# Kernel tuning notes

Measured on AMD Instinct MI355X. Metric: run time of the kernel, lower is better.

Reference implementation:

```python
import jax, jax.numpy as jnp
import numpy as np

B, S, HS = 2, 2048, 4096
NH, NKV = 32, 32
HD = HS // NH
INTER = 11008
VOCAB = 32000
EPS = 1e-6
ROPE_BASE = 10000.0


def setup_inputs() -> dict:
    key = jax.random.key(0)
    ks = jax.random.split(key, 16)
    sc = 0.02
    return {
        "hidden_states": jax.random.normal(ks[0], (B, S, HS), jnp.float32),
        "input_ids": jax.random.randint(ks[1], (B, S), 0, VOCAB, jnp.int32),
        "position_ids": jnp.arange(S, dtype=jnp.int32)[None, :],
        "embed": jax.random.normal(ks[2], (VOCAB, HS), jnp.float32) * sc,
        "fc_w": jax.random.normal(ks[3], (HS, 2 * HS), jnp.float32) * sc,
        "fc_b": jnp.zeros((HS,), jnp.float32),
        "q_w": jax.random.normal(ks[4], (NH * HD, HS), jnp.float32) * sc,
        "k_w": jax.random.normal(ks[5], (NKV * HD, HS), jnp.float32) * sc,
        "v_w": jax.random.normal(ks[6], (NKV * HD, HS), jnp.float32) * sc,
        "o_w": jax.random.normal(ks[7], (HS, NH * HD), jnp.float32) * sc,
        "gate_w": jax.random.normal(ks[8], (INTER, HS), jnp.float32) * sc,
        "up_w": jax.random.normal(ks[9], (INTER, HS), jnp.float32) * sc,
        "down_w": jax.random.normal(ks[10], (HS, INTER), jnp.float32) * sc,
        "post_ln_w": jnp.ones((HS,), jnp.float32),
    }


def _rotate_half(x):
    x1, x2 = jnp.split(x, 2, axis=-1)
    return jnp.concatenate((-x2, x1), axis=-1)


def _rms_norm(x, w, eps=EPS):
    x32 = x.astype(jnp.float32)
    x32 = x32 * jax.lax.rsqrt(jnp.mean(x32 * x32, axis=-1, keepdims=True) + eps)
    return (w * x32).astype(x.dtype)


def _forward(hidden_states, input_ids, position_ids, embed, fc_w, fc_b,
             q_w, k_w, v_w, o_w, gate_w, up_w, down_w, post_ln_w):
    # Embedding lookup (detached in original via no_grad)
    embeds = jax.lax.stop_gradient(embed[input_ids])  # [B,S,HS]
    h = jnp.concatenate((embeds, hidden_states), axis=-1) @ fc_w.T + fc_b  # [B,S,HS]

    # --- decoder layer 0 (no input_layernorm) ---
    residual = h
    q = (h @ q_w.T).reshape(B, S, NH, HD).transpose(0, 2, 1, 3)   # [B,NH,S,HD]
    k = (h @ k_w.T).reshape(B, S, NKV, HD).transpose(0, 2, 1, 3)
    v = (h @ v_w.T).reshape(B, S, NKV, HD).transpose(0, 2, 1, 3)

    # RoPE
    pos = position_ids[0].astype(jnp.float32)                      # [S]
    inv_freq = 1.0 / (ROPE_BASE ** (jnp.arange(0, HD, 2, dtype=jnp.float32) / HD))
    freqs = pos[:, None] * inv_freq[None, :]                       # [S,HD/2]
    emb = jnp.concatenate((freqs, freqs), axis=-1)                 # [S,HD]
    cos = jnp.cos(emb)[None, None, :, :]
    sin = jnp.sin(emb)[None, None, :, :]
    q = q * cos + _rotate_half(q) * sin
    k = k * cos + _rotate_half(k) * sin

    # attention (num_kv_groups == 1 here)
    scores = jnp.einsum('bhqd,bhkd->bhqk', q, k) / np.sqrt(HD)     # [B,NH,S,S]
    causal = jnp.triu(jnp.ones((S, S), bool), 1)
    scores = jnp.where(causal[None, None], -jnp.inf, scores)
    attn = jax.nn.softmax(scores.astype(jnp.float32), axis=-1).astype(q.dtype)
    out = jnp.einsum('bhqk,bhkd->bhqd', attn, v)                   # [B,NH,S,HD]
    out = out.transpose(0, 2, 1, 3).reshape(B, S, HS)
    attn_out = out @ o_w.T

    h = residual + attn_out
    residual = h
    hn = _rms_norm(h, post_ln_w)
    mlp = (jax.nn.silu(hn @ gate_w.T) * (hn @ up_w.T)) @ down_w.T
    return residual + mlp


def reference(hidden_states, input_ids, position_ids, embed, fc_w, fc_b,
              q_w, k_w, v_w, o_w, gate_w, up_w, down_w, post_ln_w):
    return _forward(hidden_states, input_ids, position_ids, embed, fc_w, fc_b,
                    q_w, k_w, v_w, o_w, gate_w, up_w, down_w, post_ln_w)
```

## Files before the change

### kernel.cpp

```cpp
#include <hip/hip_runtime.h>
#include <hip/hip_bf16.h>

typedef __attribute__((ext_vector_type(8))) short short8;
typedef __attribute__((ext_vector_type(4))) short short4v;
typedef __attribute__((ext_vector_type(4))) float floatx4;

#define B_SZ 2
#define S_SZ 2048
#define HS_SZ 4096
#define NH_SZ 32
#define HD_SZ 128
#define INTER_SZ 11008
#define M_TOT 4096
#define QKV_N 12288
#define GU_N 22016

__device__ __forceinline__ float b2f(short s){
  unsigned int u = ((unsigned int)(unsigned short)s) << 16;
  return __builtin_bit_cast(float, u);
}
__device__ __forceinline__ short f2b(float f){
  unsigned int u = __builtin_bit_cast(unsigned int, f);
  u = (u + 0x7FFFu + ((u >> 16) & 1u)) >> 16;
  return (short)u;
}

typedef __attribute__((address_space(1))) const unsigned int gu32;
typedef __attribute__((address_space(3))) unsigned int lu32;
__device__ __forceinline__ void gl2lds16(const short* g, short* l){
  __builtin_amdgcn_global_load_lds((gu32*)g, (lu32*)l, 16, 0, 0);
}

#define BARRIER() asm volatile("s_barrier" ::: "memory")
#define WAITV8()  asm volatile("s_waitcnt vmcnt(8)" ::: "memory")
#define WAITV4()  asm volatile("s_waitcnt vmcnt(4)" ::: "memory")
#define WAITV2()  asm volatile("s_waitcnt vmcnt(2)" ::: "memory")
#define WAITV0()  asm volatile("s_waitcnt vmcnt(0)" ::: "memory")

__global__ void cvt_bf16_kernel(const float* __restrict__ src, short* __restrict__ dst, long n8){
  long idx = (long)blockIdx.x * blockDim.x + threadIdx.x;
  if (idx >= n8) return;
  long e = idx * 8;
  floatx4 v0 = *(const floatx4*)(src + e);
  floatx4 v1 = *(const floatx4*)(src + e + 4);
  short8 o;
  o[0]=f2b(v0[0]); o[1]=f2b(v0[1]); o[2]=f2b(v0[2]); o[3]=f2b(v0[3]);
  o[4]=f2b(v1[0]); o[5]=f2b(v1[1]); o[6]=f2b(v1[2]); o[7]=f2b(v1[3]);
  *(short8*)(dst + e) = o;
}

__global__ void embed_concat_kernel(const float* __restrict__ hidden,
                                    const int* __restrict__ ids,
                                    const float* __restrict__ embed,
                                    short* __restrict__ X0){
  long idx = (long)blockIdx.x * blockDim.x + threadIdx.x;
  const long total = (long)M_TOT * (2*HS_SZ) / 4;
  if (idx >= total) return;
  long e = idx * 4;
  int m = (int)(e / (2*HS_SZ));
  int c = (int)(e % (2*HS_SZ));
  const float* src;
  if (c < HS_SZ){
    src = embed + (long)ids[m]*HS_SZ + c;
  } else {
    src = hidden + (long)m*HS_SZ + (c - HS_SZ);
  }
  floatx4 v = *(const floatx4*)src;
  short4v o;
  o[0]=f2b(v[0]); o[1]=f2b(v[1]); o[2]=f2b(v[2]); o[3]=f2b(v[3]);
  *(short4v*)(X0 + e) = o;
}

#define G_STAGE(op,h,kof,qb) { \
  gl2lds16(gs[op][h] + (kof), lds + (qb) + (op)*16384 + (h)*8192 + wid*1024); \
  gl2lds16(gs[op][h] + k8o[op] + (kof), lds + (qb) + (op)*16384 + (h)*8192 + wid*1024 + 512); }

#define LD_A(Mh,pb) { \
  _Pragma("unroll") \
  for (int mf=0; mf<4; mf++) \
    _Pragma("unroll") \
    for (int ks=0; ks<2; ks++) \
      af[mf][ks] = *(const short8*)(lds + (pb) + ((Mh)*128 + wr2*64 + mf*16 + lr)*64 + (((ks*4+lk)^lr7))*8); }

#define LD_B(BB,Nh,pb) { \
  _Pragma("unroll") \
  for (int nf=0; nf<2; nf++) \
    _Pragma("unroll") \
    for (int ks=0; ks<2; ks++) \
      BB[nf][ks] = *(const short8*)(lds + (pb) + 16384 + ((Nh)*128 + wc2*32 + nf*16 + lr)*64 + (((ks*4+lk)^lr7))*8); }

#define MMQ(Mh,Nh,BB) { \
  __builtin_amdgcn_s_setprio(1); \
  _Pragma("unroll") \
  for (int mf=0; mf<4; mf++) \
    _Pragma("unroll") \
    for (int nf=0; nf<2; nf++){ \
      acc[Mh][Nh][mf][nf] = __builtin_amdgcn_mfma_f32_16x16x32_bf16(af[mf][0], BB[nf][0], acc[Mh][Nh][mf][nf], 0,0,0); \
      acc[Mh][Nh][mf][nf] = __builtin_amdgcn_mfma_f32_16x16x32_bf16(af[mf][1], BB[nf][1], acc[Mh][Nh][mf][nf], 0,0,0); \
    } \
  __builtin_amdgcn_s_setprio(0); }

template<int EPI>
__global__ __launch_bounds__(512, 2)
void gemm256_kernel(const short* __restrict__ A, const short* __restrict__ Bw,
                    const short* __restrict__ Bw2, int nsplit,
                    int K, int lda, int ldc,
                    const float* __restrict__ bias,
                    const short* __restrict__ residb,
                    short* __restrict__ Cbf,
                    float* __restrict__ Cf){
  __shared__ __align__(16) short lds[65536];
  const int tid = threadIdx.x;
  const int wid = tid >> 6;
  const int lane = tid & 63;
  const int wr2 = wid >> 2, wc2 = wid & 3;
  const int lr = lane & 15, lk = lane >> 4;
  const int lr7 = lr & 7;

  const int nwg = gridDim.x * gridDim.y;
  const int id  = blockIdx.y * gridDim.x + blockIdx.x;
  const int cpx = nwg >> 3;
  const int sw  = (id & 7) * cpx + (id >> 3);
  const int bx  = sw % gridDim.x;
  const int by  = sw / gridDim.x;
  const int m0 = bx * 256, n0 = by * 256;

  const int srow = lane >> 3;
  const int sslot = (lane & 7) ^ srow;
  const long k8o[2] = { 8L * lda, 8L * K };
  const short* gs[2][2];
  #pragma unroll
  for (int h=0; h<2; h++){
    const int rowa = m0 + h*128 + wid*16 + srow;
    gs[0][h] = A + (long)rowa*lda + sslot*8;
    const int rowb = n0 + h*128 + wid*16 + srow;
    gs[1][h] = (rowb < nsplit ? Bw + (long)rowb*K
                              : Bw2 + (long)(rowb - nsplit)*K) + sslot*8;
  }

  floatx4 acc[2][2][4][2] = {};
  short8 af[4][2], b0[2][2], b1[2][2];
  const int nt = K >> 6;

  G_STAGE(0,0,0,0); G_STAGE(1,0,0,0); G_STAGE(1,1,0,0); G_STAGE(0,1,0,0);
  WAITV4(); BARRIER();

  for (int t = 0; t < nt-1; ++t){
    const int pb = (t & 1) << 15;
    const int qb = pb ^ 32768;
    const long kof = (long)(t+1) * 64;
    LD_A(0,pb); LD_B(b0,0,pb);
    G_STAGE(0,0,kof,qb);
    BARRIER();
    MMQ(0,0,b0);
    WAITV4(); BARRIER();
    LD_B(b1,1,pb);
    G_STAGE(1,0,kof,qb);
    BARRIER();
    MMQ(0,1,b1);
    WAITV4(); BARRIER();
    LD_A(1,pb);
    G_STAGE(1,1,kof,qb);
    BARRIER();
    MMQ(1,1,b1);
    BARRIER();
    G_STAGE(0,1,kof,qb);
    BARRIER();
    MMQ(1,0,b0);
    WAITV4(); BARRIER();
  }
  {
    const int pb = ((nt-1) & 1) << 15;
    LD_A(0,pb); LD_B(b0,0,pb);
    BARRIER(); MMQ(0,0,b0);
    WAITV2(); BARRIER();
    LD_B(b1,1,pb);
    BARRIER(); MMQ(0,1,b1);
    WAITV0(); BARRIER();
    LD_A(1,pb);
    BARRIER(); MMQ(1,1,b1);
    BARRIER();
    MMQ(1,0,b0);
  }

  #pragma unroll
  for (int Mh=0; Mh<2; Mh++){
    #pragma unroll
    for (int Nh=0; Nh<2; Nh++){
      #pragma unroll
      for (int mf=0; mf<4; mf++){
        #pragma unroll
        for (int nf=0; nf<2; nf++){
          const int col = n0 + Nh*128 + wc2*32 + nf*16 + lr;
          float bcol = (EPI==1) ? bias[col] : 0.0f;
          #pragma unroll
          for (int r=0; r<4; r++){
            const int row = m0 + Mh*128 + wr2*64 + mf*16 + lk*4 + r;
            float v = acc[Mh][Nh][mf][nf][r] + bcol;
            if (EPI==2 || EPI==3) v += b2f(residb[(long)row*ldc + col]);
            if (EPI==3) Cf[(long)row*ldc + col] = v;
            else        Cbf[(long)row*ldc + col] = f2b(v);
          }
        }
      }
    }
  }
}

__global__ void rope_kernel(short* __restrict__ qkv, const int* __restrict__ pos_ids){
  long idx = (long)blockIdx.x * blockDim.x + threadIdx.x;
  const long total = (long)M_TOT * NH_SZ * (HD_SZ/2);
  if (idx >= total) return;
  int i  = (int)(idx & 63);
  long rh = idx >> 6;
  int h  = (int)(rh & 31);
  int m  = (int)(rh >> 5);
  int s  = m & (S_SZ - 1);
  float p = (float)pos_ids[s];
  const float L2_10000 = 13.28771237954945f;
  float inv = exp2f(-(2.0f*i/(float)HD_SZ) * L2_10000);
  float fr = p * inv;
  float sn, cs;
  sincosf(fr, &sn, &cs);
  short* qp = qkv + (long)m*QKV_N + h*HD_SZ;
  short* kp = qp + HS_SZ;
  float q1=b2f(qp[i]), q2=b2f(qp[i+64]);
  qp[i]    = f2b(q1*cs - q2*sn);
  qp[i+64] = f2b(q2*cs + q1*sn);
  float k1=b2f(kp[i]), k2=b2f(kp[i+64]);
  kp[i]    = f2b(k1*cs - k2*sn);
  kp[i+64] = f2b(k2*cs + k1*sn);
}

__global__ __launch_bounds__(256)
void vtrans_kernel(const short* __restrict__ QKV, short* __restrict__ VT){
  __shared__ short tile[64][68];
  const int s0 = blockIdx.x * 64;
  const int d0 = blockIdx.y * 64;
  const int bh = blockIdx.z;
  const int b = bh >> 5, h = bh & 31;
  const int tid = threadIdx.x;
  #pragma unroll
  for (int it=0; it<2; it++){
    int e = (it*256 + tid) * 8;
    int ss = e >> 6, col = e & 63;
    short8 v = *(const short8*)(QKV + ((long)(b*S_SZ + s0 + ss))*QKV_N + 2*HS_SZ + h*HD_SZ + d0 + col);
    #pragma unroll
    for (int j=0;j<8;j++) tile[ss][col+j] = v[j];
  }
  __syncthreads();
  #pragma unroll
  for (int it=0; it<2; it++){
    int e = (it*256 + tid) * 8;
    int dd = e >> 6, scol = e & 63;
    short8 w;
    #pragma unroll
    for (int j=0;j<8;j++) w[j] = tile[scol+j][dd];
    *(short8*)(VT + ((long)(bh*HD_SZ + d0 + dd))*S_SZ + s0 + scol) = w;
  }
}

__global__ __launch_bounds__(512,1)
void attn_kernel(const short* __restrict__ QKV, const short* __restrict__ VT,
                 short* __restrict__ O){
  constexpr int LPD = 72;
  __shared__ __align__(16) short lds[32768];
  __shared__ __align__(16) short p_lds[8][16*LPD];
  const int bh = blockIdx.y;
  const int b = bh >> 5, h = bh & 31;
  const int qblk = blockIdx.x * 128;
  const int tid = threadIdx.x, wid = tid>>6, lane = tid&63;
  const int lr = lane & 15, lk = lane >> 4;
  const float scale = 0.08838834764831845f;

  const short* qbase = QKV + ((long)(b*S_SZ + qblk + wid*16))*QKV_N + h*HD_SZ;
  short8 qf[4];
  #pragma unroll
  for (int t=0;t<4;t++)
    qf[t] = *(const short8*)(qbase + (long)lr*QKV_N + t*32 + lk*8);

  const short* kb[2]; const short* vb[2];
  int kloff[2], vloff[2];
  #pragma unroll
  for (int p=0;p<2;p++){
    const int i = wid*2 + p;
    const int rowk = i*4 + (lane >> 4);
    const int slotk = (lane & 15) ^ (rowk & 15);
    kb[p] = QKV + ((long)(b*S_SZ) + rowk)*QKV_N + HS_SZ + h*HD_SZ + slotk*8;
    kloff[p] = i*512;
    const int dv = i*8 + (lane >> 3);
    const int slotv = (lane & 7) ^ (dv & 7);
    vb[p] = VT + ((long)(bh*HD_SZ + dv))*S_SZ + slotv*8;
    vloff[p] = 8192 + i*512;
  }

  floatx4 oacc[8] = {};
  float m_run[4] = {-1e30f,-1e30f,-1e30f,-1e30f};
  float l_run[4] = {0.f,0.f,0.f,0.f};

  const int nt = 2*(blockIdx.x + 1);

  #pragma unroll
  for (int p=0;p<2;p++){
    gl2lds16(kb[p], lds + kloff[p]);
    gl2lds16(vb[p], lds + vloff[p]);
  }

  for (int t=0; t<nt; ++t){
    const int dbase = (t & 1) * 16384;
    const int nbase = ((t+1) & 1) * 16384;
    if (t+1 < nt){
      const long kkn = (long)(t+1)*64*QKV_N;
      const long vkn = (long)(t+1)*64;
      #pragma unroll
      for (int p=0;p<2;p++){
        gl2lds16(kb[p] + kkn, lds + nbase + kloff[p]);
        gl2lds16(vb[p] + vkn, lds + nbase + vloff[p]);
      }
      WAITV4();
    } else {
      WAITV0();
    }
    BARRIER();
    const int kv0 = t*64;
    floatx4 sfr[4];
    __builtin_amdgcn_s_setprio(1);
    #pragma unroll
    for (int fn=0; fn<4; fn++){
      floatx4 s = {0.f,0.f,0.f,0.f};
      const int row = fn*16 + lr;
      #pragma unroll
      for (int tq=0; tq<4; tq++){
        short8 kf = *(const short8*)(lds + dbase + row*128 + (((tq*4+lk)^lr)&15)*8);
        s = __builtin_amdgcn_mfma_f32_16x16x32_bf16(qf[tq], kf, s, 0,0,0);
      }
      sfr[fn] = s;
    }
    __builtin_amdgcn_s_setprio(0);
    float pv[4][4];
    #pragma unroll
    for (int fn=0; fn<4; fn++){
      const int col = kv0 + fn*16 + lr;
      #pragma unroll
      for (int r=0;r<4;r++){
        const int row = qblk + wid*16 + lk*4 + r;
        float sv = sfr[fn][r] * scale;
        pv[fn][r] = (col > row) ? -1e30f : sv;
      }
    }
    float mr4[4];
    int small = 1;
    #pragma unroll
    for (int r=0;r<4;r++){
      float mr = fmaxf(fmaxf(pv[0][r], pv[1][r]), fmaxf(pv[2][r], pv[3][r]));
      mr = fmaxf(mr, __shfl_xor(mr, 1, 16));
      mr = fmaxf(mr, __shfl_xor(mr, 2, 16));
      mr = fmaxf(mr, __shfl_xor(mr, 4, 16));
      mr = fmaxf(mr, __shfl_xor(mr, 8, 16));
      mr4[r] = mr;
      small &= (mr <= m_run[r] + 8.0f) ? 1 : 0;
    }
    const int skip = __all(small);
    float alpha_[4];
    #pragma unroll
    for (int r=0;r<4;r++){
      float mnew = skip ? m_run[r] : fmaxf(m_run[r], mr4[r]);
      alpha_[r] = skip ? 1.0f : __expf(m_run[r] - mnew);
      m_run[r] = mnew;
      float rs = 0.f;
      #pragma unroll
      for (int fn=0; fn<4; fn++){
        float e = __expf(pv[fn][r] - mnew);
        p_lds[wid][(lk*4+r)*LPD + fn*16 + lr] = f2b(e);
        rs += e;
      }
      rs += __shfl_xor(rs, 1, 16);
      rs += __shfl_xor(rs, 2, 16);
      rs += __shfl_xor(rs, 4, 16);
      rs += __shfl_xor(rs, 8, 16);
      l_run[r] = l_run[r]*alpha_[r] + rs;
    }
    if (!skip){
      #pragma unroll
      for (int f=0; f<8; f++){
        #pragma unroll
        for (int r=0;r<4;r++) oacc[f][r] *= alpha_[r];
      }
    }
    short8 pf[2];
    #pragma unroll
    for (int tp=0; tp<2; tp++)
      pf[tp] = *(const short8*)(&p_lds[wid][lr*LPD + tp*32 + lk*8]);
    __builtin_amdgcn_s_setprio(1);
    #pragma unroll
    for (int f=0; f<8; f++){
      const int vrow = f*16 + lr;
      #pragma unroll
      for (int tp=0; tp<2; tp++){
        short8 vf = *(const short8*)(lds + dbase + 8192 + vrow*64 + (((tp*4+lk)^(lr&7))&7)*8);
        oacc[f] = __builtin_amdgcn_mfma_f32_16x16x32_bf16(pf[tp], vf, oacc[f], 0,0,0);
      }
    }
    __builtin_amdgcn_s_setprio(0);
    BARRIER();
  }
  #pragma unroll
  for (int r=0;r<4;r++){
    const float inv = 1.0f / l_run[r];
    const long row = (long)(b*S_SZ + qblk + wid*16 + lk*4 + r);
    #pragma unroll
    for (int f=0; f<8; f++){
      O[row*HS_SZ + h*HD_SZ + f*16 + lr] = f2b(oacc[f][r]*inv);
    }
  }
}

__global__ void rmsnorm_kernel(const short* __restrict__ X, const float* __restrict__ W,
                               short* __restrict__ Y){
  const int row = blockIdx.x;
  const short* x = X + (long)row*HS_SZ;
  float ss = 0.f;
  for (int c = threadIdx.x*8; c < HS_SZ; c += 256*8){
    short8 v = *(const short8*)(x + c);
    #pragma unroll
    for (int j=0;j<8;j++){ float f = b2f(v[j]); ss += f*f; }
  }
  ss += __shfl_xor(ss, 32); ss += __shfl_xor(ss, 16);
  ss += __shfl_xor(ss, 8);  ss += __shfl_xor(ss, 4);
  ss += __shfl_xor(ss, 2);  ss += __shfl_xor(ss, 1);
  __shared__ float red[4];
  if ((threadIdx.x & 63) == 0) red[threadIdx.x >> 6] = ss;
  __syncthreads();
  ss = red[0] + red[1] + red[2] + red[3];
  const float rs = rsqrtf(ss / (float)HS_SZ + 1e-6f);
  for (int c = threadIdx.x*8; c < HS_SZ; c += 256*8){
    short8 v = *(const short8*)(x + c);
    floatx4 w0 = *(const floatx4*)(W + c);
    floatx4 w1 = *(const floatx4*)(W + c + 4);
    short8 o;
    #pragma unroll
    for (int j=0;j<4;j++) o[j]   = f2b(b2f(v[j])  *rs*w0[j]);
    #pragma unroll
    for (int j=0;j<4;j++) o[4+j] = f2b(b2f(v[4+j])*rs*w1[j]);
    *(short8*)(Y + (long)row*HS_SZ + c) = o;
  }
}

__global__ void silu_mul_kernel(short* __restrict__ GU){
  long idx = (long)blockIdx.x * blockDim.x + threadIdx.x;
  const long total = (long)M_TOT * INTER_SZ / 8;
  if (idx >= total) return;
  long e = idx * 8;
  int m = (int)(e / INTER_SZ);
  int i = (int)(e - (long)m*INTER_SZ);
  long gix = (long)m*GU_N + i;
  short8 g = *(short8*)(GU + gix);
  short8 u = *(const short8*)(GU + gix + INTER_SZ);
  short8 o;
  #pragma unroll
  for (int j=0;j<8;j++){
    float gf = b2f(g[j]);
    float uf = b2f(u[j]);
    float s = gf / (1.0f + __expf(-gf));
    o[j] = f2b(s * uf);
  }
  *(short8*)(GU + gix) = o;
}

extern "C" void kernel_launch(void* const* d_in, const int* in_sizes, int n_in,
                              void* d_out, int out_size, void* d_ws, size_t ws_size,
                              hipStream_t stream){
  (void)in_sizes; (void)n_in; (void)out_size;
  const float* hidden = (const float*)d_in[0];
  const int*   ids    = (const int*)d_in[1];
  const int*   pos    = (const int*)d_in[2];
  const float* embed  = (const float*)d_in[3];
  const float* fc_w   = (const float*)d_in[4];
  const float* fc_b   = (const float*)d_in[5];
  const float* q_w    = (const float*)d_in[6];
  const float* k_w    = (const float*)d_in[7];
  const float* v_w    = (const float*)d_in[8];
  const float* o_w    = (const float*)d_in[9];
  const float* gate_w = (const float*)d_in[10];
  const float* up_w   = (const float*)d_in[11];
  const float* down_w = (const float*)d_in[12];
  const float* ln_w   = (const float*)d_in[13];

  char* ws = (char*)d_ws;
  size_t off = 0;
  auto alloc = [&](size_t bytes)->char*{
    char* p = ws + off;
    off = (off + bytes + 255) & ~(size_t)255;
    return p;
  };
  short* wbf   = (short*)alloc((size_t)INTER_SZ*HS_SZ*2);
  short* X0    = (short*)alloc((size_t)M_TOT*2*HS_SZ*2);
  short* h_bf  = (short*)alloc((size_t)M_TOT*HS_SZ*2);
  short* qkv_bf= (short*)alloc((size_t)M_TOT*QKV_N*2);
  short* vt_bf = (short*)alloc((size_t)M_TOT*HS_SZ*2);
  short* a_bf  = (short*)alloc((size_t)M_TOT*HS_SZ*2);
  short* h2_bf = (short*)alloc((size_t)M_TOT*HS_SZ*2);
  short* hn_bf = (short*)alloc((size_t)M_TOT*HS_SZ*2);
  short* gu_bf = (short*)alloc((size_t)M_TOT*GU_N*2);
  if (ws_size < off) return;

  short* wqkv   = gu_bf;
  short* wgate  = X0;

  auto cvt = [&](const float* src, short* dst, long n){
    long n8 = n / 8;
    cvt_bf16_kernel<<<(int)((n8 + 255)/256), 256, 0, stream>>>(src, dst, n8);
  };

  embed_concat_kernel<<<32768, 256, 0, stream>>>(hidden, ids, embed, X0);

  cvt(fc_w, wbf, (long)HS_SZ*2*HS_SZ);
  gemm256_kernel<1><<<dim3(16,16), 512, 0, stream>>>(X0, wbf, nullptr, 1<<30,
                                                     2*HS_SZ, 2*HS_SZ, HS_SZ,
                                                     fc_b, nullptr, h_bf, nullptr);
  cvt(q_w, wqkv,                       (long)HS_SZ*HS_SZ);
  cvt(k_w, wqkv + (long)HS_SZ*HS_SZ,   (long)HS_SZ*HS_SZ);
  cvt(v_w, wqkv + 2L*HS_SZ*HS_SZ,      (long)HS_SZ*HS_SZ);
  gemm256_kernel<0><<<dim3(16,48), 512, 0, stream>>>(h_bf, wqkv, nullptr, 1<<30,
                                                     HS_SZ, HS_SZ, QKV_N,
                                                     nullptr, nullptr, qkv_bf, nullptr);
  rope_kernel<<<32768, 256, 0, stream>>>(qkv_bf, pos);
  vtrans_kernel<<<dim3(S_SZ/64, HD_SZ/64, B_SZ*NH_SZ), 256, 0, stream>>>(qkv_bf, vt_bf);
  attn_kernel<<<dim3(S_SZ/128, B_SZ*NH_SZ), 512, 0, stream>>>(qkv_bf, vt_bf, a_bf);
  cvt(o_w, wbf, (long)HS_SZ*HS_SZ);
  gemm256_kernel<2><<<dim3(16,16), 512, 0, stream>>>(a_bf, wbf, nullptr, 1<<30,
                                                     HS_SZ, HS_SZ, HS_SZ,
                                                     nullptr, h_bf, h2_bf, nullptr);
  rmsnorm_kernel<<<M_TOT, 256, 0, stream>>>(h2_bf, ln_w, hn_bf);
  cvt(gate_w, wgate, (long)INTER_SZ*HS_SZ);
  cvt(up_w,   wbf,   (long)INTER_SZ*HS_SZ);
  gemm256_kernel<0><<<dim3(16,86), 512, 0, stream>>>(hn_bf, wgate, wbf, INTER_SZ,
                                                     HS_SZ, HS_SZ, GU_N,
                                                     nullptr, nullptr, gu_bf, nullptr);
  silu_mul_kernel<<<22016, 256, 0, stream>>>(gu_bf);
  cvt(down_w, wbf, (long)HS_SZ*INTER_SZ);
  gemm256_kernel<3><<<dim3(16,16), 512, 0, stream>>>(gu_bf, wbf, nullptr, 1<<30,
                                                     INTER_SZ, GU_N, HS_SZ,
                                                     nullptr, h2_bf, nullptr, (float*)d_out);
}
```

Baseline: 2.260 ms.

## Fuse SiLU-mul into gate/up GEMM epilogue via interleaved weights; vectorize RoPE

Gate and up weights are converted into a row-interleaved bf16 matrix, so adjacent output columns of the fused GEMM hold gate and up for the same intermediate index. A new epilogue variant computes silu(gate)*up with a lane shuffle and writes the half-width activation directly. This removes the separate silu_mul pass and the full-width GU intermediate write and read. RoPE is also changed to process four elements per thread with vector loads. The epilogue now idles half the lanes on stores and needs an extra workspace buffer.

Result: slower. 2.309 ms (+2.2%).

```diff
diff --git a/kernel.cpp b/kernel.cpp
--- a/kernel.cpp
+++ b/kernel.cpp
@@ -47,6 +47,32 @@
   o[0]=f2b(v0[0]); o[1]=f2b(v0[1]); o[2]=f2b(v0[2]); o[3]=f2b(v0[3]);
   o[4]=f2b(v1[0]); o[5]=f2b(v1[1]); o[6]=f2b(v1[2]); o[7]=f2b(v1[3]);
   *(short8*)(dst + e) = o;
+}
+
+__global__ void cvt_gu_kernel(const float* __restrict__ g, const float* __restrict__ u,
+                              short* __restrict__ dst){
+  long idx = (long)blockIdx.x * blockDim.x + threadIdx.x;
+  const long n8 = (long)INTER_SZ * HS_SZ / 8;
+  if (idx >= n8) return;
+  long e = idx * 8;
+  long row = e / HS_SZ;
+  long c = e - row*HS_SZ;
+  {
+    floatx4 v0 = *(const floatx4*)(g + e);
+    floatx4 v1 = *(const floatx4*)(g + e + 4);
+    short8 o;
+    o[0]=f2b(v0[0]); o[1]=f2b(v0[1]); o[2]=f2b(v0[2]); o[3]=f2b(v0[3]);
+    o[4]=f2b(v1[0]); o[5]=f2b(v1[1]); o[6]=f2b(v1[2]); o[7]=f2b(v1[3]);
+    *(short8*)(dst + (2*row)*HS_SZ + c) = o;
+  }
+  {
+    floatx4 v0 = *(const floatx4*)(u + e);
+    floatx4 v1 = *(const floatx4*)(u + e + 4);
+    short8 o;
+    o[0]=f2b(v0[0]); o[1]=f2b(v0[1]); o[2]=f2b(v0[2]); o[3]=f2b(v0[3]);
+    o[4]=f2b(v1[0]); o[5]=f2b(v1[1]); o[6]=f2b(v1[2]); o[7]=f2b(v1[3]);
+    *(short8*)(dst + (2*row+1)*HS_SZ + c) = o;
+  }
 }
 
 __global__ void embed_concat_kernel(const float* __restrict__ hidden,
@@ -197,9 +223,17 @@
           for (int r=0; r<4; r++){
             const int row = m0 + Mh*128 + wr2*64 + mf*16 + lk*4 + r;
             float v = acc[Mh][Nh][mf][nf][r] + bcol;
-            if (EPI==2 || EPI==3) v += b2f(residb[(long)row*ldc + col]);
-            if (EPI==3) Cf[(long)row*ldc + col] = v;
-            else        Cbf[(long)row*ldc + col] = f2b(v);
+            if (EPI==4){
+              float uu = __shfl_xor(v, 1);
+              if ((lr & 1) == 0){
+                float s = v / (1.0f + __expf(-v));
+                Cbf[(long)row*ldc + (col>>1)] = f2b(s*uu);
+              }
+            } else {
+              if (EPI==2 || EPI==3) v += b2f(residb[(long)row*ldc + col]);
+              if (EPI==3) Cf[(long)row*ldc + col] = v;
+              else        Cbf[(long)row*ldc + col] = f2b(v);
+            }
           }
         }
       }
@@ -209,27 +243,35 @@
 
 __global__ void rope_kernel(short* __restrict__ qkv, const int* __restrict__ pos_ids){
   long idx = (long)blockIdx.x * blockDim.x + threadIdx.x;
-  const long total = (long)M_TOT * NH_SZ * (HD_SZ/2);
+  const long total = (long)M_TOT * NH_SZ * 16;
   if (idx >= total) return;
-  int i  = (int)(idx & 63);
-  long rh = idx >> 6;
+  int i4 = (int)(idx & 15);
+  long rh = idx >> 4;
   int h  = (int)(rh & 31);
   int m  = (int)(rh >> 5);
   int s  = m & (S_SZ - 1);
   float p = (float)pos_ids[s];
   const float L2_10000 = 13.28771237954945f;
-  float inv = exp2f(-(2.0f*i/(float)HD_SZ) * L2_10000);
-  float fr = p * inv;
-  float sn, cs;
-  sincosf(fr, &sn, &cs);
-  short* qp = qkv + (long)m*QKV_N + h*HD_SZ;
+  short* qp = qkv + (long)m*QKV_N + h*HD_SZ + i4*4;
   short* kp = qp + HS_SZ;
-  float q1=b2f(qp[i]), q2=b2f(qp[i+64]);
-  qp[i]    = f2b(q1*cs - q2*sn);
-  qp[i+64] = f2b(q2*cs + q1*sn);
-  float k1=b2f(kp[i]), k2=b2f(kp[i+64]);
-  kp[i]    = f2b(k1*cs - k2*sn);
-  kp[i+64] = f2b(k2*cs + k1*sn);
+  short4v q1 = *(short4v*)qp, q2 = *(short4v*)(qp+64);
+  short4v k1 = *(short4v*)kp, k2 = *(short4v*)(kp+64);
+  short4v q1o, q2o, k1o, k2o;
+  #pragma unroll
+  for (int j=0;j<4;j++){
+    int i = i4*4 + j;
+    float inv = exp2f(-(2.0f*i/(float)HD_SZ) * L2_10000);
+    float sn, cs;
+    sincosf(p*inv, &sn, &cs);
+    float a1=b2f(q1[j]), a2=b2f(q2[j]);
+    q1o[j] = f2b(a1*cs - a2*sn);
+    q2o[j] = f2b(a2*cs + a1*sn);
+    float b1v=b2f(k1[j]), b2v=b2f(k2[j]);
+    k1o[j] = f2b(b1v*cs - b2v*sn);
+    k2o[j] = f2b(b2v*cs + b1v*sn);
+  }
+  *(short4v*)qp = q1o; *(short4v*)(qp+64) = q2o;
+  *(short4v*)kp = k1o; *(short4v*)(kp+64) = k2o;
 }
 
 __global__ __launch_bounds__(256)
@@ -444,27 +486,6 @@
     for (int j=0;j<4;j++) o[4+j] = f2b(b2f(v[4+j])*rs*w1[j]);
     *(short8*)(Y + (long)row*HS_SZ + c) = o;
   }
-}
-
-__global__ void silu_mul_kernel(short* __restrict__ GU){
-  long idx = (long)blockIdx.x * blockDim.x + threadIdx.x;
-  const long total = (long)M_TOT * INTER_SZ / 8;
-  if (idx >= total) return;
-  long e = idx * 8;
-  int m = (int)(e / INTER_SZ);
-  int i = (int)(e - (long)m*INTER_SZ);
-  long gix = (long)m*GU_N + i;
-  short8 g = *(short8*)(GU + gix);
-  short8 u = *(const short8*)(GU + gix + INTER_SZ);
-  short8 o;
-  #pragma unroll
-  for (int j=0;j<8;j++){
-    float gf = b2f(g[j]);
-    float uf = b2f(u[j]);
-    float s = gf / (1.0f + __expf(-gf));
-    o[j] = f2b(s * uf);
-  }
-  *(short8*)(GU + gix) = o;
 }
 
 extern "C" void kernel_launch(void* const* d_in, const int* in_sizes, int n_in,
@@ -494,6 +515,7 @@
     return p;
   };
   short* wbf   = (short*)alloc((size_t)INTER_SZ*HS_SZ*2);
+  short* wgu   = (short*)alloc((size_t)GU_N*HS_SZ*2);
   short* X0    = (short*)alloc((size_t)M_TOT*2*HS_SZ*2);
   short* h_bf  = (short*)alloc((size_t)M_TOT*HS_SZ*2);
   short* qkv_bf= (short*)alloc((size_t)M_TOT*QKV_N*2);
@@ -501,11 +523,10 @@
   short* a_bf  = (short*)alloc((size_t)M_TOT*HS_SZ*2);
   short* h2_bf = (short*)alloc((size_t)M_TOT*HS_SZ*2);
   short* hn_bf = (short*)alloc((size_t)M_TOT*HS_SZ*2);
-  short* gu_bf = (short*)alloc((size_t)M_TOT*GU_N*2);
   if (ws_size < off) return;
 
-  short* wqkv   = gu_bf;
-  short* wgate  = X0;
+  short* wqkv = wgu;
+  short* act  = qkv_bf;
 
   auto cvt = [&](const float* src, short* dst, long n){
     long n8 = n / 8;
@@ -524,7 +545,7 @@
   gemm256_kernel<0><<<dim3(16,48), 512, 0, stream>>>(h_bf, wqkv, nullptr, 1<<30,
                                                      HS_SZ, HS_SZ, QKV_N,
                                                      nullptr, nullptr, qkv_bf, nullptr);
-  rope_kernel<<<32768, 256, 0, stream>>>(qkv_bf, pos);
+  rope_kernel<<<8192, 256, 0, stream>>>(qkv_bf, pos);
   vtrans_kernel<<<dim3(S_SZ/64, HD_SZ/64, B_SZ*NH_SZ), 256, 0, stream>>>(qkv_bf, vt_bf);
   attn_kernel<<<dim3(S_SZ/128, B_SZ*NH_SZ), 512, 0, stream>>>(qkv_bf, vt_bf, a_bf);
   cvt(o_w, wbf, (long)HS_SZ*HS_SZ);
@@ -532,14 +553,12 @@
                                                      HS_SZ, HS_SZ, HS_SZ,
                                                      nullptr, h_bf, h2_bf, nullptr);
   rmsnorm_kernel<<<M_TOT, 256, 0, stream>>>(h2_bf, ln_w, hn_bf);
-  cvt(gate_w, wgate, (long)INTER_SZ*HS_SZ);
-  cvt(up_w,   wbf,   (long)INTER_SZ*HS_SZ);
-  gemm256_kernel<0><<<dim3(16,86), 512, 0, stream>>>(hn_bf, wgate, wbf, INTER_SZ,
-                                                     HS_SZ, HS_SZ, GU_N,
-                                                     nullptr, nullptr, gu_bf, nullptr);
-  silu_mul_kernel<<<22016, 256, 0, stream>>>(gu_bf);
+  cvt_gu_kernel<<<22016, 256, 0, stream>>>(gate_w, up_w, wgu);
+  gemm256_kernel<4><<<dim3(16,86), 512, 0, stream>>>(hn_bf, wgu, nullptr, 1<<30,
+                                                     HS_SZ, HS_SZ, INTER_SZ,
+                                                     nullptr, nullptr, act, nullptr);
   cvt(down_w, wbf, (long)HS_SZ*INTER_SZ);
-  gemm256_kernel<3><<<dim3(16,16), 512, 0, stream>>>(gu_bf, wbf, nullptr, 1<<30,
-                                                     INTER_SZ, GU_N, HS_SZ,
+  gemm256_kernel<3><<<dim3(16,16), 512, 0, stream>>>(act, wbf, nullptr, 1<<30,
+                                                     INTER_SZ, INTER_SZ, HS_SZ,
                                                      nullptr, h2_bf, nullptr, (float*)d_out);
 }
```
